# Kernel optimization log

Hardware: AMD Instinct MI355X
Metric: run time of the kernel (lower is better)

## Reference

```python
import jax, jax.numpy as jnp
import numpy as np

NEG = -9e15

def setup_inputs() -> dict:
    key = jax.random.key(0)
    k1, k2, k3, k4 = jax.random.split(key, 4)
    N, F_IN, F_OUT = 8192, 256, 256
    h = jax.random.normal(k1, (N, F_IN), dtype=jnp.float32)
    adj = jax.random.randint(k2, (N, N), 0, 2, dtype=jnp.int32)
    W = jax.random.normal(k3, (F_IN, F_OUT), dtype=jnp.float32) * (1.0 / np.sqrt(F_IN))
    a = jax.random.normal(k4, (2 * F_OUT,), dtype=jnp.float32) * (1.0 / np.sqrt(2 * F_OUT))
    return {"h": h, "adj": adj, "W": W, "a": a}

def reference(h, adj, W, a):
    # Wh: [N, F_out]
    Wh = h @ W
    F_OUT = Wh.shape[1]
    a1, a2 = a[:F_OUT], a[F_OUT:]
    # cat-based score decomposes: e_ij = leaky_relu(a1.Wh_i + a2.Wh_j)
    s1 = Wh @ a1  # [N]
    s2 = Wh @ a2  # [N]
    e = jax.nn.leaky_relu(s1[:, None] + s2[None, :], negative_slope=0.2)  # [N, N]
    e = jnp.where(adj > 0, e, NEG)
    attention = jax.nn.softmax(e, axis=-1)
    # dropout is identity in eval mode
    return attention @ Wh
```

## Files before the change

### kernel.cpp

```cpp
#include <hip/hip_runtime.h>

typedef short s8v  __attribute__((ext_vector_type(8)));
typedef float f4v  __attribute__((ext_vector_type(4)));
typedef int   v4i  __attribute__((ext_vector_type(4)));
typedef float v4f  __attribute__((ext_vector_type(4)));
typedef int   v2i  __attribute__((ext_vector_type(2)));

#define NNODES 8192
#define FDIM   256
#define NJC    4
#define JLEN   2048
#define TROWS  64
#define KSTEP  32
#define NSTEP  64
#define RSTR   ((size_t)16 * NNODES)

__device__ __forceinline__ unsigned short f2bf(float f) {
    unsigned int x = __builtin_bit_cast(unsigned int, f);
    x += 0x7fffu + ((x >> 16) & 1u);
    return (unsigned short)(x >> 16);
}
__device__ __forceinline__ int cvt_pk(float lo, float hi) {
    int r;
    asm("v_cvt_pk_bf16_f32 %0, %1, %2" : "=v"(r) : "v"(lo), "v"(hi));
    return r;
}

__global__ __launch_bounds__(256) void prep_kernel(const float* __restrict__ W,
                                                   const float* __restrict__ a,
                                                   unsigned short* __restrict__ WT,
                                                   float* __restrict__ v1,
                                                   float* __restrict__ v2) {
    if (blockIdx.x < 256) {
        int idx = blockIdx.x * 256 + threadIdx.x;
        int r = idx >> 8, c = idx & 255;
        WT[c * 256 + r] = f2bf(W[r * 256 + c]);
    } else {
        __shared__ float r1[256], r2[256];
        int b = blockIdx.x - 256, n = threadIdx.x;
        float w = W[(size_t)b * FDIM + n];
        r1[n] = w * a[n];
        r2[n] = w * a[FDIM + n];
        __syncthreads();
        for (int off = 128; off > 0; off >>= 1) {
            if (n < off) { r1[n] += r1[n + off]; r2[n] += r2[n + off]; }
            __syncthreads();
        }
        if (n == 0) { v1[b] = r1[0]; v2[b] = r2[0]; }
    }
}

__global__ __launch_bounds__(128) void wh_kernel(
    const float* __restrict__ h, const unsigned short* __restrict__ WT,
    const float* __restrict__ v1, const float* __restrict__ v2,
    unsigned short* __restrict__ PB,
    float* __restrict__ s1, float* __restrict__ s2)
{
    __shared__ float v1_lds[FDIM], v2_lds[FDIM];
    int tid = threadIdx.x;
    v1_lds[tid] = v1[tid];       v1_lds[tid + 128] = v1[tid + 128];
    v2_lds[tid] = v2[tid];       v2_lds[tid + 128] = v2[tid + 128];
    __syncthreads();

    int w = tid >> 6, lane = tid & 63, q = lane >> 4, l15 = lane & 15;
    int i_base = blockIdx.x * 32 + w * 16;

    f4v acc[16] = {};
    float s1p = 0.f, s2p = 0.f;

    for (int k0 = 0; k0 < 256; k0 += 32) {
        const float* hp = h + (size_t)(i_base + l15) * FDIM + k0 + q * 8;
        f4v h0 = *(const f4v*)hp;
        f4v h1 = *(const f4v*)(hp + 4);
        union { v4i u; s8v s; } af;
        af.u[0] = cvt_pk(h0[0], h0[1]);
        af.u[1] = cvt_pk(h0[2], h0[3]);
        af.u[2] = cvt_pk(h1[0], h1[1]);
        af.u[3] = cvt_pk(h1[2], h1[3]);
#pragma unroll
        for (int j = 0; j < 4; ++j) {
            s1p += h0[j] * v1_lds[k0 + q * 8 + j] + h1[j] * v1_lds[k0 + q * 8 + 4 + j];
            s2p += h0[j] * v2_lds[k0 + q * 8 + j] + h1[j] * v2_lds[k0 + q * 8 + 4 + j];
        }
#pragma unroll
        for (int t = 0; t < 16; ++t) {
            s8v bf = *(const s8v*)(WT + (size_t)(t * 16 + l15) * FDIM + k0 + q * 8);
            acc[t] = __builtin_amdgcn_mfma_f32_16x16x32_bf16(af.s, bf, acc[t], 0, 0, 0);
        }
    }

    s1p += __shfl_xor(s1p, 16, 64);
    s1p += __shfl_xor(s1p, 32, 64);
    s2p += __shfl_xor(s2p, 16, 64);
    s2p += __shfl_xor(s2p, 32, 64);
    if (lane < 16) {
        s1[i_base + lane] = s1p;
        s2[i_base + lane] = s2p;
    }

#pragma unroll
    for (int t = 0; t < 16; ++t) {
        int i0 = i_base + q * 4;
        size_t a16 = (size_t)((i0 >> 5) * 16 + t) * 512
                   + l15 * 32 + ((i0 >> 3) & 3) * 8 + (i0 & 7);
        v2i pk;
        pk[0] = cvt_pk(acc[t][0], acc[t][1]);
        pk[1] = cvt_pk(acc[t][2], acc[t][3]);
        *(v2i*)(PB + a16) = pk;
    }
}

__global__ __launch_bounds__(256, 2) void attn_partial(
    const int* __restrict__ adj, const unsigned short* __restrict__ PB,
    const float* __restrict__ s1, const float* __restrict__ s2,
    float* __restrict__ Npart, float* __restrict__ dpart)
{
    __shared__ float s2_lds[JLEN];

    int tid = threadIdx.x;
    int jc = blockIdx.x & 3, rt = blockIdx.x >> 2;
    int j0 = jc * JLEN;

    for (int i = tid; i < JLEN / 4; i += 256)
        ((v4f*)s2_lds)[i] = ((const v4f*)(s2 + j0))[i];

    int g = tid >> 6, lane = tid & 63, q = lane >> 4, l15 = lane & 15;

    float s1r[4];
#pragma unroll
    for (int rh = 0; rh < 4; ++rh) s1r[rh] = s1[rt * TROWS + rh * 16 + l15];

    const unsigned short* pbb = PB + (size_t)(jc * NSTEP) * 16 * 512 + l15 * 32 + q * 8;
    const int* arow = adj + (size_t)(rt * TROWS + l15) * NNODES + j0 + q * 8;

    f4v acc[4][4] = {};
    float dsum4[4] = {0.f, 0.f, 0.f, 0.f};

    __syncthreads();

    v4i aA[4][2], aB[4][2];
#pragma unroll
    for (int rh = 0; rh < 4; ++rh) {
        const int* pp = arow + rh * RSTR;
        aA[rh][0] = *(const v4i*)(pp);
        aA[rh][1] = *(const v4i*)(pp + 4);
        aB[rh][0] = *(const v4i*)(pp + KSTEP);
        aB[rh][1] = *(const v4i*)(pp + KSTEP + 4);
    }
    s8v bfA[4], bfB[4];
#pragma unroll
    for (int t = 0; t < 4; ++t)
        bfA[t] = *(const s8v*)(pbb + (size_t)(g * 4 + t) * 512);

#define ASTEP(S, AC, BC, BN) do {                                             \
    int sc = (S);                                                             \
    v4f svA = *(const v4f*)&s2_lds[sc * KSTEP + q * 8];                       \
    v4f svB = *(const v4f*)&s2_lds[sc * KSTEP + q * 8 + 4];                   \
    int sb = (sc + 1 < NSTEP) ? sc + 1 : 0;                                   \
    _Pragma("unroll")                                                         \
    for (int t = 0; t < 4; ++t)                                               \
        BN[t] = *(const s8v*)(pbb + (size_t)(sb * 16 + g * 4 + t) * 512);     \
    int sn = (sc + 2 < NSTEP) ? sc + 2 : 0;                                   \
    _Pragma("unroll")                                                         \
    for (int rh = 0; rh < 4; ++rh) {                                          \
        float pa[8];                                                          \
        _Pragma("unroll")                                                     \
        for (int j = 0; j < 4; ++j) {                                         \
            float x = s1r[rh] + svA[j];                                       \
            pa[j] = (AC[rh][0][j] > 0) ? __expf(fmaxf(x, 0.2f * x)) : 0.0f;   \
            float x2 = s1r[rh] + svB[j];                                      \
            pa[4 + j] = (AC[rh][1][j] > 0) ? __expf(fmaxf(x2, 0.2f * x2)) : 0.0f; \
            dsum4[rh] += pa[j] + pa[4 + j];                                   \
        }                                                                     \
        union { v4i u; s8v s; } af;                                           \
        af.u[0] = cvt_pk(pa[0], pa[1]);  af.u[1] = cvt_pk(pa[2], pa[3]);      \
        af.u[2] = cvt_pk(pa[4], pa[5]);  af.u[3] = cvt_pk(pa[6], pa[7]);      \
        _Pragma("unroll")                                                     \
        for (int t = 0; t < 4; ++t)                                           \
            acc[rh][t] = __builtin_amdgcn_mfma_f32_16x16x32_bf16(af.s, BC[t], acc[rh][t], 0, 0, 0); \
        const int* pp = arow + rh * RSTR + (size_t)sn * KSTEP;                \
        AC[rh][0] = *(const v4i*)(pp);                                        \
        AC[rh][1] = *(const v4i*)(pp + 4);                                    \
    }                                                                         \
} while (0)

    for (int s = 0; s < NSTEP; s += 2) {
        ASTEP(s,     aA, bfA, bfB);
        ASTEP(s + 1, aB, bfB, bfA);
    }
#undef ASTEP

#pragma unroll
    for (int rh = 0; rh < 4; ++rh) {
        dsum4[rh] += __shfl_xor(dsum4[rh], 16, 64);
        dsum4[rh] += __shfl_xor(dsum4[rh], 32, 64);
    }
    if (g == 0 && lane < 16) {
#pragma unroll
        for (int rh = 0; rh < 4; ++rh)
            dpart[jc * NNODES + rt * TROWS + rh * 16 + lane] = dsum4[rh];
    }

#pragma unroll
    for (int rh = 0; rh < 4; ++rh)
#pragma unroll
        for (int r = 0; r < 4; ++r) {
            int row = rh * 16 + q * 4 + r;
            float* base = Npart + ((size_t)(jc * NNODES) + rt * TROWS + row) * FDIM;
#pragma unroll
            for (int t = 0; t < 4; ++t)
                __builtin_nontemporal_store(acc[rh][t][r], base + g * 64 + t * 16 + l15);
        }
}

__global__ __launch_bounds__(256) void reduce_kernel(
    const float* __restrict__ Npart, const float* __restrict__ dpart,
    float* __restrict__ out)
{
    int i = blockIdx.x, n = threadIdx.x;
    float d = 0.f, acc = 0.f;
#pragma unroll
    for (int jc = 0; jc < NJC; ++jc) {
        d += dpart[jc * NNODES + i];
        acc += Npart[((size_t)(jc * NNODES) + i) * FDIM + n];
    }
    out[(size_t)i * FDIM + n] = acc / fmaxf(d, 1e-30f);
}

extern "C" void kernel_launch(void* const* d_in, const int* in_sizes, int n_in,
                              void* d_out, int out_size, void* d_ws, size_t ws_size,
                              hipStream_t stream) {
    const float* h   = (const float*)d_in[0];
    const int*   adj = (const int*)d_in[1];
    const float* W   = (const float*)d_in[2];
    const float* a   = (const float*)d_in[3];
    float* out = (float*)d_out;

    char* ws = (char*)d_ws;
    unsigned short* PB = (unsigned short*)ws;
    float* s1 = (float*)(ws + (4u << 20));
    float* s2 = (float*)(ws + (4u << 20) + (32u << 10));
    unsigned short* WT = (unsigned short*)(ws + (4u << 20) + (64u << 10));
    float* v1 = (float*)(ws + (4u << 20) + (192u << 10));
    float* v2 = (float*)(ws + (4u << 20) + (193u << 10));
    float* dpart = (float*)(ws + (5u << 20));
    float* Npart = (float*)(ws + (8u << 20));

    hipLaunchKernelGGL(prep_kernel, dim3(512), dim3(256), 0, stream, W, a, WT, v1, v2);
    hipLaunchKernelGGL(wh_kernel, dim3(256), dim3(128), 0, stream, h, WT, v1, v2, PB, s1, s2);
    hipLaunchKernelGGL(attn_partial, dim3(128 * NJC), dim3(256), 0, stream,
                       adj, PB, s1, s2, Npart, dpart);
    hipLaunchKernelGGL(reduce_kernel, dim3(NNODES), dim3(256), 0, stream, Npart, dpart, out);
}
```

Baseline: 489.5 us.

## Factor exp of leaky-relu score into precomputed row/column exponentials, halve row tile

Replaces the per-element exp(leaky_relu(s1+s2)) with products of precomputed exponentials: exp(s1)*exp(s2) when the positive branch applies, else exp(0.2 s1)*exp(0.2 s2). The column factors are precomputed into LDS and the row factors into registers. This removes the transcendental from the inner loop. The row tile also shrinks from 64 to 32 with occupancy raised to 4 blocks per CU, doubling the grid, so each block re-reads the shared PB operands more often. The factored products can overflow or lose precision for large scores, since no max subtraction is done.

```diff
diff --git a/kernel.cpp b/kernel.cpp
--- a/kernel.cpp
+++ b/kernel.cpp
@@ -10,7 +10,7 @@
 #define FDIM   256
 #define NJC    4
 #define JLEN   2048
-#define TROWS  64
+#define TROWS  32
 #define KSTEP  32
 #define NSTEP  64
 #define RSTR   ((size_t)16 * NNODES)
@@ -24,6 +24,13 @@
     int r;
     asm("v_cvt_pk_bf16_f32 %0, %1, %2" : "=v"(r) : "v"(lo), "v"(hi));
     return r;
+}
+
+__device__ __forceinline__ float pel(float e1, float f1, float e2, float f2, int ad) {
+    float pp = e1 * e2;
+    float pn = f1 * f2;
+    float s  = (pp > 1.0f) ? pp : pn;
+    return (ad > 0) ? s : 0.0f;
 }
 
 __global__ __launch_bounds__(256) void prep_kernel(const float* __restrict__ W,
@@ -110,42 +117,49 @@
     }
 }
 
-__global__ __launch_bounds__(256, 2) void attn_partial(
+__global__ __launch_bounds__(256, 4) void attn_partial(
     const int* __restrict__ adj, const unsigned short* __restrict__ PB,
     const float* __restrict__ s1, const float* __restrict__ s2,
     float* __restrict__ Npart, float* __restrict__ dpart)
 {
-    __shared__ float s2_lds[JLEN];
+    __shared__ float s2ef[JLEN * 2];
 
     int tid = threadIdx.x;
     int jc = blockIdx.x & 3, rt = blockIdx.x >> 2;
     int j0 = jc * JLEN;
 
-    for (int i = tid; i < JLEN / 4; i += 256)
-        ((v4f*)s2_lds)[i] = ((const v4f*)(s2 + j0))[i];
+    for (int i = tid; i < JLEN; i += 256) {
+        float x = s2[j0 + i];
+        s2ef[2 * i]     = __expf(x);
+        s2ef[2 * i + 1] = __expf(0.2f * x);
+    }
 
     int g = tid >> 6, lane = tid & 63, q = lane >> 4, l15 = lane & 15;
 
-    float s1r[4];
-#pragma unroll
-    for (int rh = 0; rh < 4; ++rh) s1r[rh] = s1[rt * TROWS + rh * 16 + l15];
+    float E1[2], F1[2];
+#pragma unroll
+    for (int rh = 0; rh < 2; ++rh) {
+        float s1v = s1[rt * TROWS + rh * 16 + l15];
+        E1[rh] = __expf(s1v);
+        F1[rh] = __expf(0.2f * s1v);
+    }
 
     const unsigned short* pbb = PB + (size_t)(jc * NSTEP) * 16 * 512 + l15 * 32 + q * 8;
     const int* arow = adj + (size_t)(rt * TROWS + l15) * NNODES + j0 + q * 8;
 
-    f4v acc[4][4] = {};
-    float dsum4[4] = {0.f, 0.f, 0.f, 0.f};
+    f4v acc[2][4] = {};
+    float ds[2] = {0.f, 0.f};
 
     __syncthreads();
 
-    v4i aA[4][2], aB[4][2];
-#pragma unroll
-    for (int rh = 0; rh < 4; ++rh) {
+    v4i aC[2][2], aN[2][2];
+#pragma unroll
+    for (int rh = 0; rh < 2; ++rh) {
         const int* pp = arow + rh * RSTR;
-        aA[rh][0] = *(const v4i*)(pp);
-        aA[rh][1] = *(const v4i*)(pp + 4);
-        aB[rh][0] = *(const v4i*)(pp + KSTEP);
-        aB[rh][1] = *(const v4i*)(pp + KSTEP + 4);
+        aC[rh][0] = *(const v4i*)(pp);
+        aC[rh][1] = *(const v4i*)(pp + 4);
+        aN[rh][0] = *(const v4i*)(pp + KSTEP);
+        aN[rh][1] = *(const v4i*)(pp + KSTEP + 4);
     }
     s8v bfA[4], bfB[4];
 #pragma unroll
@@ -154,55 +168,58 @@
 
 #define ASTEP(S, AC, BC, BN) do {                                             \
     int sc = (S);                                                             \
-    v4f svA = *(const v4f*)&s2_lds[sc * KSTEP + q * 8];                       \
-    v4f svB = *(const v4f*)&s2_lds[sc * KSTEP + q * 8 + 4];                   \
     int sb = (sc + 1 < NSTEP) ? sc + 1 : 0;                                   \
     _Pragma("unroll")                                                         \
     for (int t = 0; t < 4; ++t)                                               \
         BN[t] = *(const s8v*)(pbb + (size_t)(sb * 16 + g * 4 + t) * 512);     \
     int sn = (sc + 2 < NSTEP) ? sc + 2 : 0;                                   \
+    const float* efp = &s2ef[(sc * KSTEP + q * 8) * 2];                       \
+    v4f e01 = *(const v4f*)(efp);                                             \
+    v4f e23 = *(const v4f*)(efp + 4);                                         \
+    v4f e45 = *(const v4f*)(efp + 8);                                         \
+    v4f e67 = *(const v4f*)(efp + 12);                                        \
     _Pragma("unroll")                                                         \
-    for (int rh = 0; rh < 4; ++rh) {                                          \
-        float pa[8];                                                          \
-        _Pragma("unroll")                                                     \
-        for (int j = 0; j < 4; ++j) {                                         \
-            float x = s1r[rh] + svA[j];                                       \
-            pa[j] = (AC[rh][0][j] > 0) ? __expf(fmaxf(x, 0.2f * x)) : 0.0f;   \
-            float x2 = s1r[rh] + svB[j];                                      \
-            pa[4 + j] = (AC[rh][1][j] > 0) ? __expf(fmaxf(x2, 0.2f * x2)) : 0.0f; \
-            dsum4[rh] += pa[j] + pa[4 + j];                                   \
-        }                                                                     \
+    for (int rh = 0; rh < 2; ++rh) {                                          \
+        float p0 = pel(E1[rh], F1[rh], e01[0], e01[1], AC[rh][0][0]);         \
+        float p1 = pel(E1[rh], F1[rh], e01[2], e01[3], AC[rh][0][1]);         \
+        float p2 = pel(E1[rh], F1[rh], e23[0], e23[1], AC[rh][0][2]);         \
+        float p3 = pel(E1[rh], F1[rh], e23[2], e23[3], AC[rh][0][3]);         \
+        float p4 = pel(E1[rh], F1[rh], e45[0], e45[1], AC[rh][1][0]);         \
+        float p5 = pel(E1[rh], F1[rh], e45[2], e45[3], AC[rh][1][1]);         \
+        float p6 = pel(E1[rh], F1[rh], e67[0], e67[1], AC[rh][1][2]);         \
+        float p7 = pel(E1[rh], F1[rh], e67[2], e67[3], AC[rh][1][3]);         \
+        ds[rh] += ((p0 + p1) + (p2 + p3)) + ((p4 + p5) + (p6 + p7));          \
         union { v4i u; s8v s; } af;                                           \
-        af.u[0] = cvt_pk(pa[0], pa[1]);  af.u[1] = cvt_pk(pa[2], pa[3]);      \
-        af.u[2] = cvt_pk(pa[4], pa[5]);  af.u[3] = cvt_pk(pa[6], pa[7]);      \
+        af.u[0] = cvt_pk(p0, p1);  af.u[1] = cvt_pk(p2, p3);                  \
+        af.u[2] = cvt_pk(p4, p5);  af.u[3] = cvt_pk(p6, p7);                  \
         _Pragma("unroll")                                                     \
         for (int t = 0; t < 4; ++t)                                           \
             acc[rh][t] = __builtin_amdgcn_mfma_f32_16x16x32_bf16(af.s, BC[t], acc[rh][t], 0, 0, 0); \
-        const int* pp = arow + rh * RSTR + (size_t)sn * KSTEP;                \
-        AC[rh][0] = *(const v4i*)(pp);                                        \
-        AC[rh][1] = *(const v4i*)(pp + 4);                                    \
+        const int* pp2 = arow + rh * RSTR + (size_t)sn * KSTEP;               \
+        AC[rh][0] = *(const v4i*)(pp2);                                       \
+        AC[rh][1] = *(const v4i*)(pp2 + 4);                                   \
     }                                                                         \
 } while (0)
 
     for (int s = 0; s < NSTEP; s += 2) {
-        ASTEP(s,     aA, bfA, bfB);
-        ASTEP(s + 1, aB, bfB, bfA);
+        ASTEP(s,     aC, bfA, bfB);
+        ASTEP(s + 1, aN, bfB, bfA);
     }
 #undef ASTEP
 
 #pragma unroll
-    for (int rh = 0; rh < 4; ++rh) {
-        dsum4[rh] += __shfl_xor(dsum4[rh], 16, 64);
-        dsum4[rh] += __shfl_xor(dsum4[rh], 32, 64);
+    for (int rh = 0; rh < 2; ++rh) {
+        ds[rh] += __shfl_xor(ds[rh], 16, 64);
+        ds[rh] += __shfl_xor(ds[rh], 32, 64);
     }
     if (g == 0 && lane < 16) {
 #pragma unroll
-        for (int rh = 0; rh < 4; ++rh)
-            dpart[jc * NNODES + rt * TROWS + rh * 16 + lane] = dsum4[rh];
-    }
-
-#pragma unroll
-    for (int rh = 0; rh < 4; ++rh)
+        for (int rh = 0; rh < 2; ++rh)
+            dpart[jc * NNODES + rt * TROWS + rh * 16 + lane] = ds[rh];
+    }
+
+#pragma unroll
+    for (int rh = 0; rh < 2; ++rh)
 #pragma unroll
         for (int r = 0; r < 4; ++r) {
             int row = rh * 16 + q * 4 + r;
@@ -248,7 +265,7 @@
 
     hipLaunchKernelGGL(prep_kernel, dim3(512), dim3(256), 0, stream, W, a, WT, v1, v2);
     hipLaunchKernelGGL(wh_kernel, dim3(256), dim3(128), 0, stream, h, WT, v1, v2, PB, s1, s2);
-    hipLaunchKernelGGL(attn_partial, dim3(128 * NJC), dim3(256), 0, stream,
+    hipLaunchKernelGGL(attn_partial, dim3((NNODES / TROWS) * NJC), dim3(256), 0, stream,
                        adj, PB, s1, s2, Npart, dpart);
     hipLaunchKernelGGL(reduce_kernel, dim3(NNODES), dim3(256), 0, stream, Npart, dpart, out);
 }
```

Result: slower. 540.8 us (+10.5%).
